# Kernel tuning notes

Hardware: AMD Instinct MI355X
Metric: run time of the kernel (lower is better)

The kernel has to match this reference:

```python
import jax, jax.numpy as jnp
import numpy as np
import math

B, S, HID = 2, 2048, 1024
D = 64            # size_per_head
H = HID // D      # num heads = 16
ROT = 32          # rotary_hsize = size_per_head // 2


def _apply_rotary(qk, sinusoids):
    # qk: [B, S, H, D]; sinusoids: [B, 2, S, ROT]
    sin = sinusoids[:, 0, :, None, :]   # [B, S, 1, ROT]
    cos = sinusoids[:, 1, :, None, :]
    qk_rope = qk[..., :ROT]
    # torch.stack([-a[..., ::2], a[..., 1::2]], -1).reshape(a.shape)
    rot2 = jnp.stack([-qk_rope[..., ::2], qk_rope[..., 1::2]], axis=-1).reshape(qk_rope.shape)
    qk_rope = qk_rope * cos + rot2 * sin
    return jnp.concatenate([qk_rope, qk[..., ROT:]], axis=-1)


def setup_inputs() -> dict:
    key = jax.random.key(0)
    ks = jax.random.split(key, 8)
    sc = 1.0 / math.sqrt(HID)
    return {
        "x": jax.random.normal(ks[0], (B, S, HID), jnp.float32),
        "sinusoids": jax.random.normal(ks[1], (B, 2, S, ROT), jnp.float32),
        "attention_bias": jax.random.uniform(ks[2], (B, 1, S, S), jnp.float32),
        "Wq": jax.random.normal(ks[3], (HID, HID), jnp.float32) * sc,
        "bq": jnp.zeros((HID,), jnp.float32),
        "Wk": jax.random.normal(ks[4], (HID, HID), jnp.float32) * sc,
        "bk": jnp.zeros((HID,), jnp.float32),
        "Wv": jax.random.normal(ks[5], (HID, HID), jnp.float32) * sc,
        "bv": jnp.zeros((HID,), jnp.float32),
        "Wo": jax.random.normal(ks[6], (HID, HID), jnp.float32) * sc,
    }


def reference(x, sinusoids, attention_bias, Wq, bq, Wk, bk, Wv, bv, Wo):
    q = (x @ Wq + bq).reshape(B, S, H, D)
    k = (x @ Wk + bk).reshape(B, S, H, D)
    v = (x @ Wv + bv).reshape(B, S, H, D)
    # original concatenates q,k along the heads dim before rotary; since rotary
    # broadcasts over heads, applying it to each separately is identical math
    q = _apply_rotary(q, sinusoids)
    k = _apply_rotary(k, sinusoids)
    q = q / math.sqrt(D)
    scores = jnp.einsum('bqhd,bkhd->bhqk', q, k)          # [B,H,S,S]
    probs = jax.nn.softmax(scores, axis=-1)
    probs = probs * attention_bias                         # multiplicative bias AFTER softmax
    out = jnp.einsum('bhqk,bkhd->bqhd', probs, v)          # [B,S,H,D]
    out = out.reshape(B, S, HID)
    return out @ Wo
```

## Files before the change

### kernel.cpp

```cpp
#include <hip/hip_runtime.h>
#include <math.h>

#define B_   2
#define S_   2048
#define HID_ 1024
#define D_   64
#define H_   16
#define ROT_ 32
#define M_   (B_*S_)

typedef __attribute__((ext_vector_type(4))) short  short4v;
typedef __attribute__((ext_vector_type(8))) short  short8;
typedef __attribute__((ext_vector_type(4))) float  floatx4;
typedef __attribute__((ext_vector_type(16))) float floatx16;
typedef __attribute__((ext_vector_type(2))) unsigned int uint2v;

__device__ __forceinline__ unsigned short f2bf(float f) {
  unsigned int x = __builtin_bit_cast(unsigned int, f);
  x += 0x7fffu + ((x >> 16) & 1u);
  return (unsigned short)(x >> 16);
}
__device__ __forceinline__ unsigned int cvt_pk_bf16(float lo, float hi) {
  unsigned int r;
  asm("v_cvt_pk_bf16_f32 %0, %1, %2" : "=v"(r) : "v"(lo), "v"(hi));
  return r;
}
__device__ __forceinline__ void gload_lds16(const unsigned short* g, unsigned short* l) {
  __builtin_amdgcn_global_load_lds(
      (const __attribute__((address_space(1))) unsigned int*)g,
      (__attribute__((address_space(3))) unsigned int*)l, 16, 0, 0);
}

__global__ void cast_bf16(const float* __restrict__ in, unsigned short* __restrict__ out) {
  int i = (blockIdx.x * 256 + threadIdx.x) * 4;
  floatx4 v = *(const floatx4*)(in + i);
  unsigned short o[4];
  o[0] = f2bf(v[0]); o[1] = f2bf(v[1]); o[2] = f2bf(v[2]); o[3] = f2bf(v[3]);
  *(unsigned long long*)(out + i) = *(unsigned long long*)o;
}

__global__ void transW(const float* __restrict__ W0, const float* __restrict__ W1,
                       const float* __restrict__ W2, const float* __restrict__ W3,
                       unsigned short* __restrict__ T0, unsigned short* __restrict__ T1,
                       unsigned short* __restrict__ T2, unsigned short* __restrict__ T3) {
  const float* W; unsigned short* T;
  int z = blockIdx.z;
  if (z == 0)      { W = W0; T = T0; }
  else if (z == 1) { W = W1; T = T1; }
  else if (z == 2) { W = W2; T = T2; }
  else             { W = W3; T = T3; }
  __shared__ float tile[32][33];
  int bx = blockIdx.x * 32, by = blockIdx.y * 32;
  int tx = threadIdx.x, ty = threadIdx.y;
  #pragma unroll
  for (int j = 0; j < 4; j++)
    tile[ty + j*8][tx] = W[(size_t)(by + ty + j*8) * HID_ + bx + tx];
  __syncthreads();
  #pragma unroll
  for (int j = 0; j < 4; j++)
    T[(size_t)(bx + ty + j*8) * HID_ + by + tx] = f2bf(tile[tx][ty + j*8]);
}

template <int MODE>
__global__ __launch_bounds__(256) void gemm_bt(
    const unsigned short* __restrict__ A,
    const unsigned short* __restrict__ Bt0, const unsigned short* __restrict__ Bt1,
    const unsigned short* __restrict__ Bt2,
    const float* __restrict__ bias0, const float* __restrict__ bias1,
    const float* __restrict__ bias2,
    void* __restrict__ out0, void* __restrict__ out1, void* __restrict__ out2,
    const float* __restrict__ sins, float sc0)
{
  int wg = blockIdx.x + (blockIdx.y << 3) + (blockIdx.z << 8);
  int work = (wg & 7) * 96 + (wg >> 3);
  int zz = work >> 8;
  int rem = work & 255;
  int ty_ = rem >> 3, tx_ = rem & 7;

  const unsigned short* Bt; const float* bias; void* Out; float sc;
  if (zz == 0)      { Bt = Bt0; bias = bias0; Out = out0; sc = sc0; }
  else if (zz == 1) { Bt = Bt1; bias = bias1; Out = out1; sc = 1.f; }
  else              { Bt = Bt2; bias = bias2; Out = out2; sc = 1.f; }
  const int K = HID_, N = HID_;
  int m0 = ty_ * 128, n0 = tx_ * 128;
  __shared__ alignas(16) unsigned short sA[3][128 * 32];
  __shared__ alignas(16) unsigned short sB[3][128 * 32];
  int t = threadIdx.x;
  int lane = t & 63, wave = t >> 6;
  int quad = lane >> 4, l16 = lane & 15;
  int wr = wave >> 1, wc = wave & 1;

  int srow = (lane >> 2), scol = (lane & 3) * 8;
  const unsigned short* gA0 = A  + (size_t)(m0 + wave*32 +  0 + srow) * K + scol;
  const unsigned short* gA1 = A  + (size_t)(m0 + wave*32 + 16 + srow) * K + scol;
  const unsigned short* gB0 = Bt + (size_t)(n0 + wave*32 +  0 + srow) * K + scol;
  const unsigned short* gB1 = Bt + (size_t)(n0 + wave*32 + 16 + srow) * K + scol;

#define GSTAGE(bi, k0) do { \
    gload_lds16(gA0 + (k0), sA[bi] + (wave*32 +  0) * 32); \
    gload_lds16(gA1 + (k0), sA[bi] + (wave*32 + 16) * 32); \
    gload_lds16(gB0 + (k0), sB[bi] + (wave*32 +  0) * 32); \
    gload_lds16(gB1 + (k0), sB[bi] + (wave*32 + 16) * 32); \
  } while (0)

  floatx4 acc[4][4];
  #pragma unroll
  for (int i = 0; i < 4; i++)
    #pragma unroll
    for (int j = 0; j < 4; j++)
      acc[i][j] = (floatx4){0.f, 0.f, 0.f, 0.f};

  const int NK = K / 32;
  GSTAGE(0, 0);
  GSTAGE(1, 32);
  for (int ks = 0; ks < NK; ks++) {
    int cur = ks % 3;
    if (ks + 1 < NK) asm volatile("s_waitcnt vmcnt(4)" ::: "memory");
    else             asm volatile("s_waitcnt vmcnt(0)" ::: "memory");
    __builtin_amdgcn_s_barrier();
    __builtin_amdgcn_sched_barrier(0);
    if (ks + 2 < NK) GSTAGE((ks + 2) % 3, (ks + 2) * 32);

    short8 af[4], bf[4];
    #pragma unroll
    for (int i = 0; i < 4; i++) {
      af[i] = *(const short8*)(sA[cur] + (wr * 64 + i * 16 + l16) * 32 + quad * 8);
      bf[i] = *(const short8*)(sB[cur] + (wc * 64 + i * 16 + l16) * 32 + quad * 8);
    }
    #pragma unroll
    for (int i = 0; i < 4; i++)
      #pragma unroll
      for (int j = 0; j < 4; j++)
        acc[i][j] = __builtin_amdgcn_mfma_f32_16x16x32_bf16(af[i], bf[j], acc[i][j], 0, 0, 0);
  }
#undef GSTAGE

  #pragma unroll
  for (int i = 0; i < 4; i++) {
    int mbase = m0 + wr * 64 + i * 16 + quad * 4;
    #pragma unroll
    for (int j = 0; j < 4; j++) {
      int n = n0 + wc * 64 + j * 16 + l16;
      float bv = bias ? bias[n] : 0.f;
      if (MODE == 1) {
        #pragma unroll
        for (int r = 0; r < 4; r++)
          ((float*)Out)[(size_t)(mbase + r) * N + n] = acc[i][j][r] + bv;
      } else if (zz == 2) {
        int bb = mbase >> 11, ss = mbase & 2047;
        int hh = n >> 6, dd = n & 63;
        unsigned short pk[4];
        #pragma unroll
        for (int r = 0; r < 4; r++) pk[r] = f2bf(acc[i][j][r] + bv);
        *(unsigned long long*)((unsigned short*)Out +
            (((size_t)(bb * H_ + hh) * D_ + dd) * S_ + ss)) = *(unsigned long long*)pk;
      } else if (j < 2) {
        int jh = j * 16 + l16;
        #pragma unroll
        for (int r = 0; r < 4; r++) {
          int row = mbase + r, bb = row >> 11, ss = row & 2047;
          float sn = sins[((size_t)(bb * 2 + 0) * S_ + ss) * ROT_ + jh];
          float cs = sins[((size_t)(bb * 2 + 1) * S_ + ss) * ROT_ + jh];
          float f = (jh & 1) ? (cs + sn) : (cs - sn);
          ((unsigned short*)Out)[(size_t)row * N + n] = f2bf((acc[i][j][r] + bv) * f * sc);
        }
      } else {
        #pragma unroll
        for (int r = 0; r < 4; r++)
          ((unsigned short*)Out)[(size_t)(mbase + r) * N + n] = f2bf((acc[i][j][r] + bv) * sc);
      }
    }
  }
}

__global__ __launch_bounds__(256) void gemm_bt64(
    const unsigned short* __restrict__ A, const unsigned short* __restrict__ Bt,
    float* __restrict__ Out)
{
  const int K = HID_, N = HID_;
  int wg = blockIdx.x + (blockIdx.y << 4);
  int work = (wg & 7) * 64 + (wg >> 3);
  int m0 = (work >> 4) * 128, n0 = (work & 15) * 64;
  __shared__ alignas(16) unsigned short sA[3][128 * 32];
  __shared__ alignas(16) unsigned short sB[3][64 * 32];
  int t = threadIdx.x;
  int lane = t & 63, wave = t >> 6;
  int quad = lane >> 4, l16 = lane & 15;
  int wr = wave >> 1, wc = wave & 1;

  int srow = lane >> 2, scol = (lane & 3) * 8;
  const unsigned short* gA0 = A  + (size_t)(m0 + wave*32 +  0 + srow) * K + scol;
  const unsigned short* gA1 = A  + (size_t)(m0 + wave*32 + 16 + srow) * K + scol;
  const unsigned short* gB0 = Bt + (size_t)(n0 + wave*16 + srow) * K + scol;

#define GSTAGE(bi, k0) do { \
    gload_lds16(gA0 + (k0), sA[bi] + (wave*32 +  0) * 32); \
    gload_lds16(gA1 + (k0), sA[bi] + (wave*32 + 16) * 32); \
    gload_lds16(gB0 + (k0), sB[bi] + (wave*16) * 32); \
  } while (0)

  floatx4 acc[4][2];
  #pragma unroll
  for (int i = 0; i < 4; i++)
    #pragma unroll
    for (int j = 0; j < 2; j++)
      acc[i][j] = (floatx4){0.f, 0.f, 0.f, 0.f};

  const int NK = K / 32;
  GSTAGE(0, 0);
  GSTAGE(1, 32);
  for (int ks = 0; ks < NK; ks++) {
    int cur = ks % 3;
    if (ks + 1 < NK) asm volatile("s_waitcnt vmcnt(3)" ::: "memory");
    else             asm volatile("s_waitcnt vmcnt(0)" ::: "memory");
    __builtin_amdgcn_s_barrier();
    __builtin_amdgcn_sched_barrier(0);
    if (ks + 2 < NK) GSTAGE((ks + 2) % 3, (ks + 2) * 32);

    short8 af[4], bf[2];
    #pragma unroll
    for (int i = 0; i < 4; i++)
      af[i] = *(const short8*)(sA[cur] + (wr * 64 + i * 16 + l16) * 32 + quad * 8);
    #pragma unroll
    for (int j = 0; j < 2; j++)
      bf[j] = *(const short8*)(sB[cur] + (wc * 32 + j * 16 + l16) * 32 + quad * 8);
    #pragma unroll
    for (int i = 0; i < 4; i++)
      #pragma unroll
      for (int j = 0; j < 2; j++)
        acc[i][j] = __builtin_amdgcn_mfma_f32_16x16x32_bf16(af[i], bf[j], acc[i][j], 0, 0, 0);
  }
#undef GSTAGE

  #pragma unroll
  for (int i = 0; i < 4; i++) {
    int mbase = m0 + wr * 64 + i * 16 + quad * 4;
    #pragma unroll
    for (int j = 0; j < 2; j++) {
      int n = n0 + wc * 32 + j * 16 + l16;
      #pragma unroll
      for (int r = 0; r < 4; r++)
        Out[(size_t)(mbase + r) * N + n] = acc[i][j][r];
    }
  }
}

__global__ __launch_bounds__(512, 1) void attn(
    const unsigned short* __restrict__ Q, const unsigned short* __restrict__ Kb,
    const unsigned short* __restrict__ Vt, const float* __restrict__ bias,
    unsigned short* __restrict__ Out)
{
  int b = blockIdx.z, h = blockIdx.y;
  int t = threadIdx.x;
  int lane = t & 63, wave = t >> 6;
  int g = wave >> 2, wg = wave & 3;
  int l32 = lane & 31, hl = lane >> 5;
  int s7 = l32 & 7;
  int q0 = blockIdx.x * 128 + wg * 32;
  const int RS = H_ * D_;
  const int NT = S_ / 128;

  __shared__ alignas(16) unsigned short smem[65536];
  unsigned short* bg = smem + g * 32768;

  const unsigned short* Qbase = Q + ((size_t)(b * S_) * H_ + h) * D_;
  const unsigned short* Kbase = Kb + ((size_t)(b * S_) * H_ + h) * D_;
  const unsigned short* Vbase = Vt + ((size_t)(b * H_) + h) * D_ * S_;

  short8 qf[4];
  {
    const unsigned short* qp = Qbase + (size_t)(q0 + l32) * RS + 8 * hl;
    qf[0] = *(const short8*)(qp);
    qf[1] = *(const short8*)(qp + 16);
    qf[2] = *(const short8*)(qp + 32);
    qf[3] = *(const short8*)(qp + 48);
  }

  int tg = t & 255;
  int row0 = tg >> 3;
  int csw  = (tg & 7) ^ (row0 & 7);
  const unsigned short* gK0 = Kbase + (size_t)(g*1024 + row0)      * RS + csw * 8;
  const unsigned short* gK1 = Kbase + (size_t)(g*1024 + row0 + 32) * RS + csw * 8;
  const unsigned short* gV0 = Vbase + (size_t)(row0)      * S_ + g*1024 + csw * 8;
  const unsigned short* gV1 = Vbase + (size_t)(row0 + 32) * S_ + g*1024 + csw * 8;

  const float* bp = bias + (size_t)b * S_ * S_ + (size_t)(q0 + l32) * S_ + g * 1024 + 4 * hl;

#define STAGE(bi, tk) do { \
    unsigned short* kb_ = bg + (bi) * 4096; \
    unsigned short* vb_ = bg + 16384 + (bi) * 4096; \
    size_t ko_ = (size_t)(tk) * 64 * RS; int vo_ = (tk) * 64; \
    gload_lds16(gK0 + ko_, kb_ + tg * 8); \
    gload_lds16(gK1 + ko_, kb_ + (256 + tg) * 8); \
    gload_lds16(gV0 + vo_, vb_ + tg * 8); \
    gload_lds16(gV1 + vo_, vb_ + (256 + tg) * 8); \
  } while (0)

  float l_run = 0.f;
  floatx16 o0, o1;
  #pragma unroll
  for (int r = 0; r < 16; r++) { o0[r] = 0.f; o1[r] = 0.f; }

  STAGE(0, 0);
  floatx4 b0[4], b1[4];
  #pragma unroll
  for (int rg = 0; rg < 4; rg++) {
    b0[rg] = *(const floatx4*)(bp + 8 * rg);
    b1[rg] = *(const floatx4*)(bp + 32 + 8 * rg);
  }
  STAGE(1, 1);
  STAGE(2, 2);

  for (int it = 0; it < NT; ++it) {
    int cur = it & 3;
    asm volatile("s_waitcnt vmcnt(16)" ::: "memory");
    __builtin_amdgcn_s_barrier();
    __builtin_amdgcn_sched_barrier(0);
    if (it < NT - 3) STAGE((it + 3) & 3, it + 3);

    const unsigned short* kbuf = bg + cur * 4096;
    const unsigned short* vbuf = bg + 16384 + cur * 4096;
    int itn = ((it + 1) & (NT - 1)) * 64;

    floatx16 st;
    #pragma unroll
    for (int r = 0; r < 16; r++) st[r] = 0.f;
    __builtin_amdgcn_s_setprio(1);
    #pragma unroll
    for (int ks = 0; ks < 4; ks++) {
      short8 kf = *(const short8*)(kbuf + l32 * 64 + (((2 * ks + hl) ^ s7) * 8));
      st = __builtin_amdgcn_mfma_f32_32x32x16_bf16(kf, qf[ks], st, 0, 0, 0);
    }
    __builtin_amdgcn_s_setprio(0);

    short4v pf0[4];
    #pragma unroll
    for (int rg = 0; rg < 4; rg++) {
      float p0 = __builtin_amdgcn_exp2f(st[rg * 4 + 0]);
      float p1 = __builtin_amdgcn_exp2f(st[rg * 4 + 1]);
      float p2 = __builtin_amdgcn_exp2f(st[rg * 4 + 2]);
      float p3 = __builtin_amdgcn_exp2f(st[rg * 4 + 3]);
      l_run += (p0 + p1) + (p2 + p3);
      uint2v u;
      u[0] = cvt_pk_bf16(p0 * b0[rg][0], p1 * b0[rg][1]);
      u[1] = cvt_pk_bf16(p2 * b0[rg][2], p3 * b0[rg][3]);
      pf0[rg] = __builtin_bit_cast(short4v, u);
    }
    #pragma unroll
    for (int rg = 0; rg < 4; rg++)
      b0[rg] = *(const floatx4*)(bp + itn + 8 * rg);

    floatx16 st1;
    #pragma unroll
    for (int r = 0; r < 16; r++) st1[r] = 0.f;
    __builtin_amdgcn_s_setprio(1);
    #pragma unroll
    for (int ks = 0; ks < 4; ks++) {
      short8 kf = *(const short8*)(kbuf + (32 + l32) * 64 + (((2 * ks + hl) ^ s7) * 8));
      st1 = __builtin_amdgcn_mfma_f32_32x32x16_bf16(kf, qf[ks], st1, 0, 0, 0);
    }
    #pragma unroll
    for (int gg = 0; gg < 4; gg++) {
      int ch = (gg ^ s7) * 8 + hl * 4;
      short4v vf0 = *(const short4v*)(vbuf + l32 * 64 + ch);
      short4v vf1 = *(const short4v*)(vbuf + (32 + l32) * 64 + ch);
      o0 = __builtin_amdgcn_mfma_f32_32x32x8bf16_1k(pf0[gg], vf0, o0, 0, 0, 0);
      o1 = __builtin_amdgcn_mfma_f32_32x32x8bf16_1k(pf0[gg], vf1, o1, 0, 0, 0);
    }
    __builtin_amdgcn_s_setprio(0);

    short4v pf1[4];
    #pragma unroll
    for (int rg = 0; rg < 4; rg++) {
      float p0 = __builtin_amdgcn_exp2f(st1[rg * 4 + 0]);
      float p1 = __builtin_amdgcn_exp2f(st1[rg * 4 + 1]);
      float p2 = __builtin_amdgcn_exp2f(st1[rg * 4 + 2]);
      float p3 = __builtin_amdgcn_exp2f(st1[rg * 4 + 3]);
      l_run += (p0 + p1) + (p2 + p3);
      uint2v u;
      u[0] = cvt_pk_bf16(p0 * b1[rg][0], p1 * b1[rg][1]);
      u[1] = cvt_pk_bf16(p2 * b1[rg][2], p3 * b1[rg][3]);
      pf1[rg] = __builtin_bit_cast(short4v, u);
    }
    #pragma unroll
    for (int rg = 0; rg < 4; rg++)
      b1[rg] = *(const floatx4*)(bp + itn + 32 + 8 * rg);

    __builtin_amdgcn_s_setprio(1);
    #pragma unroll
    for (int gg = 0; gg < 4; gg++) {
      int ch = ((4 + gg) ^ s7) * 8 + hl * 4;
      short4v vf0 = *(const short4v*)(vbuf + l32 * 64 + ch);
      short4v vf1 = *(const short4v*)(vbuf + (32 + l32) * 64 + ch);
      o0 = __builtin_amdgcn_mfma_f32_32x32x8bf16_1k(pf1[gg], vf0, o0, 0, 0, 0);
      o1 = __builtin_amdgcn_mfma_f32_32x32x8bf16_1k(pf1[gg], vf1, o1, 0, 0, 0);
    }
    __builtin_amdgcn_s_setprio(0);
  }
#undef STAGE

  float l2 = l_run + __shfl_xor(l_run, 32);

  float* sO = (float*)smem;
  float* sL = (float*)(smem + 16384);

  __syncthreads();
  if (g == 1) {
    #pragma unroll
    for (int r = 0; r < 16; r++) {
      int ql = (r & 3) + 8 * (r >> 2) + 4 * hl;
      sO[(wg * 32 + ql) * 64 + l32]      = o0[r];
      sO[(wg * 32 + ql) * 64 + 32 + l32] = o1[r];
    }
    if (hl == 0) sL[wg * 32 + l32] = l2;
  }
  __syncthreads();
  if (g == 0) {
    float linv = __builtin_amdgcn_rcpf(l2 + sL[wg * 32 + l32]);
    #pragma unroll
    for (int r = 0; r < 16; r++) {
      int ql = (r & 3) + 8 * (r >> 2) + 4 * hl;
      float sc = __shfl(linv, ql);
      size_t base = ((size_t)(b * S_ + q0 + ql) * H_ + h) * D_;
      float a0 = o0[r] + sO[(wg * 32 + ql) * 64 + l32];
      float a1 = o1[r] + sO[(wg * 32 + ql) * 64 + 32 + l32];
      Out[base + l32]      = f2bf(a0 * sc);
      Out[base + 32 + l32] = f2bf(a1 * sc);
    }
  }
}

extern "C" void kernel_launch(void* const* d_in, const int* in_sizes, int n_in,
                              void* d_out, int out_size, void* d_ws, size_t ws_size,
                              hipStream_t stream) {
  (void)in_sizes; (void)n_in; (void)out_size; (void)ws_size;
  const float* x    = (const float*)d_in[0];
  const float* sins = (const float*)d_in[1];
  const float* ab   = (const float*)d_in[2];
  const float* Wq   = (const float*)d_in[3];
  const float* bq   = (const float*)d_in[4];
  const float* Wk   = (const float*)d_in[5];
  const float* bk   = (const float*)d_in[6];
  const float* Wv   = (const float*)d_in[7];
  const float* bv   = (const float*)d_in[8];
  const float* Wo   = (const float*)d_in[9];
  float* out = (float*)d_out;
  char* ws = (char*)d_ws;

  unsigned short* xb  = (unsigned short*)(ws);
  unsigned short* Wqt = (unsigned short*)(ws + ((size_t) 8 << 20));
  unsigned short* Wkt = (unsigned short*)(ws + ((size_t)10 << 20));
  unsigned short* Wvt = (unsigned short*)(ws + ((size_t)12 << 20));
  unsigned short* Wot = (unsigned short*)(ws + ((size_t)14 << 20));
  unsigned short* Qb  = (unsigned short*)(ws + ((size_t)16 << 20));
  unsigned short* Kb  = (unsigned short*)(ws + ((size_t)24 << 20));
  unsigned short* Vtb = (unsigned short*)(ws + ((size_t)32 << 20));
  unsigned short* Ab  = (unsigned short*)(ws + ((size_t)40 << 20));

  const float c1 = 0.125f * 1.44269504088896f;

  cast_bf16<<<dim3((M_ * HID_) / (256 * 4)), dim3(256), 0, stream>>>(x, xb);
  transW<<<dim3(32, 32, 4), dim3(32, 8), 0, stream>>>(Wq, Wk, Wv, Wo, Wqt, Wkt, Wvt, Wot);
  gemm_bt<0><<<dim3(8, 32, 3), dim3(256), 0, stream>>>(xb, Wqt, Wkt, Wvt, bq, bk, bv,
                                                       Qb, Kb, Vtb, sins, c1);
  attn<<<dim3(S_ / 128, H_, B_), dim3(512), 0, stream>>>(Qb, Kb, Vtb, ab, Ab);
  gemm_bt64<<<dim3(HID_ / 64, M_ / 128), dim3(256), 0, stream>>>(Ab, Wot, out);
}
```

Measured before the change: 257.4 us.

## Drop intra-block KV split in attention; use 256-thread blocks at 2 per CU

The attention kernel used to split the key sequence between two 4-wave groups in a 512-thread block, then merge their partial outputs through shared memory. Now each 256-thread block walks the whole key range itself, using half the LDS, and launch bounds allow two blocks per CU. This removes the cross-group reduction and its barriers, and lets two independent blocks overlap on one CU. The cost is a serial loop twice as long per block and less parallelism inside each block.

```diff
diff --git a/kernel.cpp b/kernel.cpp
--- a/kernel.cpp
+++ b/kernel.cpp
@@ -245,7 +245,7 @@
   }
 }
 
-__global__ __launch_bounds__(512, 1) void attn(
+__global__ __launch_bounds__(256, 2) void attn(
     const unsigned short* __restrict__ Q, const unsigned short* __restrict__ Kb,
     const unsigned short* __restrict__ Vt, const float* __restrict__ bias,
     unsigned short* __restrict__ Out)
@@ -253,15 +253,13 @@
   int b = blockIdx.z, h = blockIdx.y;
   int t = threadIdx.x;
   int lane = t & 63, wave = t >> 6;
-  int g = wave >> 2, wg = wave & 3;
   int l32 = lane & 31, hl = lane >> 5;
   int s7 = l32 & 7;
-  int q0 = blockIdx.x * 128 + wg * 32;
+  int q0 = blockIdx.x * 128 + wave * 32;
   const int RS = H_ * D_;
-  const int NT = S_ / 128;
-
-  __shared__ alignas(16) unsigned short smem[65536];
-  unsigned short* bg = smem + g * 32768;
+  const int NT = S_ / 64;
+
+  __shared__ alignas(16) unsigned short smem[32768];
 
   const unsigned short* Qbase = Q + ((size_t)(b * S_) * H_ + h) * D_;
   const unsigned short* Kbase = Kb + ((size_t)(b * S_) * H_ + h) * D_;
@@ -276,24 +274,23 @@
     qf[3] = *(const short8*)(qp + 48);
   }
 
-  int tg = t & 255;
-  int row0 = tg >> 3;
-  int csw  = (tg & 7) ^ (row0 & 7);
-  const unsigned short* gK0 = Kbase + (size_t)(g*1024 + row0)      * RS + csw * 8;
-  const unsigned short* gK1 = Kbase + (size_t)(g*1024 + row0 + 32) * RS + csw * 8;
-  const unsigned short* gV0 = Vbase + (size_t)(row0)      * S_ + g*1024 + csw * 8;
-  const unsigned short* gV1 = Vbase + (size_t)(row0 + 32) * S_ + g*1024 + csw * 8;
-
-  const float* bp = bias + (size_t)b * S_ * S_ + (size_t)(q0 + l32) * S_ + g * 1024 + 4 * hl;
+  int row0 = t >> 3;
+  int csw  = (t & 7) ^ (row0 & 7);
+  const unsigned short* gK0 = Kbase + (size_t)(row0)      * RS + csw * 8;
+  const unsigned short* gK1 = Kbase + (size_t)(row0 + 32) * RS + csw * 8;
+  const unsigned short* gV0 = Vbase + (size_t)(row0)      * S_ + csw * 8;
+  const unsigned short* gV1 = Vbase + (size_t)(row0 + 32) * S_ + csw * 8;
+
+  const float* bp = bias + (size_t)b * S_ * S_ + (size_t)(q0 + l32) * S_ + 4 * hl;
 
 #define STAGE(bi, tk) do { \
-    unsigned short* kb_ = bg + (bi) * 4096; \
-    unsigned short* vb_ = bg + 16384 + (bi) * 4096; \
+    unsigned short* kb_ = smem + (bi) * 4096; \
+    unsigned short* vb_ = smem + 16384 + (bi) * 4096; \
     size_t ko_ = (size_t)(tk) * 64 * RS; int vo_ = (tk) * 64; \
-    gload_lds16(gK0 + ko_, kb_ + tg * 8); \
-    gload_lds16(gK1 + ko_, kb_ + (256 + tg) * 8); \
-    gload_lds16(gV0 + vo_, vb_ + tg * 8); \
-    gload_lds16(gV1 + vo_, vb_ + (256 + tg) * 8); \
+    gload_lds16(gK0 + ko_, kb_ + t * 8); \
+    gload_lds16(gK1 + ko_, kb_ + (256 + t) * 8); \
+    gload_lds16(gV0 + vo_, vb_ + t * 8); \
+    gload_lds16(gV1 + vo_, vb_ + (256 + t) * 8); \
   } while (0)
 
   float l_run = 0.f;
@@ -318,8 +315,8 @@
     __builtin_amdgcn_sched_barrier(0);
     if (it < NT - 3) STAGE((it + 3) & 3, it + 3);
 
-    const unsigned short* kbuf = bg + cur * 4096;
-    const unsigned short* vbuf = bg + 16384 + cur * 4096;
+    const unsigned short* kbuf = smem + cur * 4096;
+    const unsigned short* vbuf = smem + 16384 + cur * 4096;
     int itn = ((it + 1) & (NT - 1)) * 64;
 
     floatx16 st;
@@ -399,34 +396,14 @@
   }
 #undef STAGE
 
-  float l2 = l_run + __shfl_xor(l_run, 32);
-
-  float* sO = (float*)smem;
-  float* sL = (float*)(smem + 16384);
-
-  __syncthreads();
-  if (g == 1) {
-    #pragma unroll
-    for (int r = 0; r < 16; r++) {
-      int ql = (r & 3) + 8 * (r >> 2) + 4 * hl;
-      sO[(wg * 32 + ql) * 64 + l32]      = o0[r];
-      sO[(wg * 32 + ql) * 64 + 32 + l32] = o1[r];
-    }
-    if (hl == 0) sL[wg * 32 + l32] = l2;
-  }
-  __syncthreads();
-  if (g == 0) {
-    float linv = __builtin_amdgcn_rcpf(l2 + sL[wg * 32 + l32]);
-    #pragma unroll
-    for (int r = 0; r < 16; r++) {
-      int ql = (r & 3) + 8 * (r >> 2) + 4 * hl;
-      float sc = __shfl(linv, ql);
-      size_t base = ((size_t)(b * S_ + q0 + ql) * H_ + h) * D_;
-      float a0 = o0[r] + sO[(wg * 32 + ql) * 64 + l32];
-      float a1 = o1[r] + sO[(wg * 32 + ql) * 64 + 32 + l32];
-      Out[base + l32]      = f2bf(a0 * sc);
-      Out[base + 32 + l32] = f2bf(a1 * sc);
-    }
+  float linv = __builtin_amdgcn_rcpf(l_run + __shfl_xor(l_run, 32));
+  #pragma unroll
+  for (int r = 0; r < 16; r++) {
+    int ql = (r & 3) + 8 * (r >> 2) + 4 * hl;
+    float sc = __shfl(linv, ql);
+    size_t base = ((size_t)(b * S_ + q0 + ql) * H_ + h) * D_;
+    Out[base + l32]      = f2bf(o0[r] * sc);
+    Out[base + 32 + l32] = f2bf(o1[r] * sc);
   }
 }
 
@@ -463,6 +440,6 @@
   transW<<<dim3(32, 32, 4), dim3(32, 8), 0, stream>>>(Wq, Wk, Wv, Wo, Wqt, Wkt, Wvt, Wot);
   gemm_bt<0><<<dim3(8, 32, 3), dim3(256), 0, stream>>>(xb, Wqt, Wkt, Wvt, bq, bk, bv,
                                                        Qb, Kb, Vtb, sins, c1);
-  attn<<<dim3(S_ / 128, H_, B_), dim3(512), 0, stream>>>(Qb, Kb, Vtb, ab, Ab);
+  attn<<<dim3(S_ / 128, H_, B_), dim3(256), 0, stream>>>(Qb, Kb, Vtb, ab, Ab);
   gemm_bt64<<<dim3(HID_ / 64, M_ / 128), dim3(256), 0, stream>>>(Ab, Wot, out);
 }
```

After: 245.3 us. -4.7%, faster.
